# Performance work log

Hardware: AMD Instinct MI355X
Metric: run time of the kernel (lower is better)

Reference implementation:

```python
import jax, jax.numpy as jnp
import numpy as np

D_MODEL = 1024
NHEAD = 16
HEAD_DIM = D_MODEL // NHEAD
NEG = -1e9
LN_EPS = 1e-5


def setup_inputs() -> dict:
    key = jax.random.key(0)
    ks = jax.random.split(key, 12)
    B, S, D = 2, 2048, D_MODEL
    scale = 1.0 / np.sqrt(D)
    inp = {
        "x": jax.random.normal(ks[0], (B, S, D), jnp.float32),
        "mask": jax.random.randint(ks[1], (B, S), 0, 2, jnp.int32),
        "wq": jax.random.normal(ks[2], (D, D), jnp.float32) * scale,
        "bq": jnp.zeros((D,), jnp.float32),
        "wk": jax.random.normal(ks[3], (D, D), jnp.float32) * scale,
        "bk": jnp.zeros((D,), jnp.float32),
        "wv": jax.random.normal(ks[4], (D, D), jnp.float32) * scale,
        "bv": jnp.zeros((D,), jnp.float32),
        "wo": jax.random.normal(ks[5], (D, D), jnp.float32) * scale,
        "bo": jnp.zeros((D,), jnp.float32),
        "attn_bias": jax.random.normal(ks[6], (1, NHEAD, 1, 1), jnp.float32) * 0.02,
        "ln_g": jnp.ones((D,), jnp.float32),
        "ln_b": jnp.zeros((D,), jnp.float32),
    }
    return inp


def _layer_norm(x, g, b):
    mu = jnp.mean(x, axis=-1, keepdims=True)
    var = jnp.var(x, axis=-1, keepdims=True)
    return (x - mu) * jax.lax.rsqrt(var + LN_EPS) * g + b


def reference(x, mask, wq, bq, wk, bk, wv, bv, wo, bo, attn_bias, ln_g, ln_b):
    B, S, D = x.shape
    H, Hd = NHEAD, HEAD_DIM
    # QKV projections -> [B, H, S, Hd]
    q = (x @ wq + bq).reshape(B, S, H, Hd).transpose(0, 2, 1, 3)
    k = (x @ wk + bk).reshape(B, S, H, Hd).transpose(0, 2, 1, 3)
    v = (x @ wv + bv).reshape(B, S, H, Hd).transpose(0, 2, 1, 3)
    # Scores [B, H, S, S] with per-head scalar bias
    scores = jnp.einsum("bhsd,bhtd->bhst", q, k) / jnp.sqrt(jnp.float32(Hd))
    scores = scores + attn_bias
    # mask [B,S] -> [B,1,1,S]; masked_fill where mask == 0
    m = (mask[:, None, None, :] == 0)
    scores = jnp.where(m, jnp.float32(NEG), scores)
    attn = jax.nn.softmax(scores, axis=-1)  # dropout = identity (eval)
    out = jnp.einsum("bhst,bhtd->bhsd", attn, v)
    out = out.transpose(0, 2, 1, 3).reshape(B, S, D)
    out = out @ wo + bo
    return _layer_norm(x + out, ln_g, ln_b)
```

## Files before the change

kernel.cpp:

```cpp
#include <hip/hip_runtime.h>

typedef __attribute__((ext_vector_type(8))) short short8;
typedef __attribute__((ext_vector_type(4))) float f32x4;
typedef __attribute__((ext_vector_type(16))) float f32x16;
typedef __attribute__((ext_vector_type(4))) unsigned short us4;

#define DEV __device__ __forceinline__

#define GLD16(gp, lp) __builtin_amdgcn_global_load_lds( \
    (const __attribute__((address_space(1))) void*)(gp), \
    (__attribute__((address_space(3))) void*)(lp), 16, 0, 0)

DEV unsigned short f2bf(float f) {
    union { float f; unsigned u; } v; v.f = f;
    unsigned r = v.u + 0x7fffu + ((v.u >> 16) & 1u);
    return (unsigned short)(r >> 16);
}

DEV float bf2f(unsigned short u) {
    union { unsigned u; float f; } v; v.u = (unsigned)u << 16;
    return v.f;
}

DEV float fexp2(float x) {
#if __has_builtin(__builtin_amdgcn_exp2f)
    return __builtin_amdgcn_exp2f(x);
#else
    return __expf(x * 0.69314718056f);
#endif
}

__global__ __launch_bounds__(256) void k_convert(const float* __restrict__ x,
                                                 unsigned short* __restrict__ xb) {
    int i = blockIdx.x * 256 + threadIdx.x;
    float4 v = ((const float4*)x)[i];
    us4 o = { f2bf(v.x), f2bf(v.y), f2bf(v.z), f2bf(v.w) };
    ((us4*)xb)[i] = o;
}

__global__ __launch_bounds__(256) void k_transw(const float* __restrict__ wq, const float* __restrict__ wk,
                                                const float* __restrict__ wv, const float* __restrict__ wo,
                                                unsigned short* __restrict__ wt) {
    __shared__ float tile[32][33];
    const int z = blockIdx.z;
    const float* src = (z == 0) ? wq : (z == 1) ? wk : (z == 2) ? wv : wo;
    unsigned short* dst = wt + (size_t)z * (1u << 20);
    const int n0 = blockIdx.x * 32, k0 = blockIdx.y * 32;
    const int tx = threadIdx.x, ty = threadIdx.y;
#pragma unroll
    for (int i = 0; i < 4; ++i)
        tile[ty + i * 8][tx] = src[(size_t)(k0 + ty + i * 8) * 1024 + n0 + tx];
    __syncthreads();
#pragma unroll
    for (int i = 0; i < 4; ++i)
        dst[(size_t)(n0 + ty + i * 8) * 1024 + k0 + tx] = f2bf(tile[tx][ty + i * 8]);
}

__global__ __launch_bounds__(256) void k_gemm_qkv(const unsigned short* __restrict__ A,
                                                  const unsigned short* __restrict__ Wt,
                                                  const float* __restrict__ bq,
                                                  const float* __restrict__ bk,
                                                  const float* __restrict__ bv,
                                                  unsigned short* __restrict__ Qo,
                                                  unsigned short* __restrict__ Ko,
                                                  unsigned short* __restrict__ Vo,
                                                  float qscale) {
    __shared__ unsigned short lA[2][128 * 32];
    __shared__ unsigned short lB[2][3][64 * 32];
    const int m0 = blockIdx.y * 128, n0 = blockIdx.x * 64;
    const int tid = threadIdx.x;
    const int lane = tid & 63;
    const int w = tid >> 6, wm = w >> 1, wn = w & 1;

    const int arow0 = tid >> 2, acl = tid & 3;
    const int arow1 = (tid + 256) >> 2;
    const int brow = tid >> 2;
    const unsigned short* agp0 = A + (size_t)(m0 + arow0) * 1024 + acl * 8;
    const unsigned short* agp1 = A + (size_t)(m0 + arow1) * 1024 + acl * 8;
    const unsigned short* bgp[3];
#pragma unroll
    for (int z = 0; z < 3; ++z)
        bgp[z] = Wt + ((size_t)z << 20) + (size_t)(n0 + brow) * 1024 + acl * 8;
    const int apc0 = ((arow0 << 2) | (acl ^ ((arow0 >> 1) & 3))) * 8;
    const int apc1 = ((arow1 << 2) | (acl ^ ((arow1 >> 1) & 3))) * 8;
    const int bpc  = ((brow  << 2) | (acl ^ ((brow  >> 1) & 3))) * 8;

    int ach[4], bch[2];
#pragma unroll
    for (int mt = 0; mt < 4; ++mt) {
        int row = wm * 64 + mt * 16 + (lane & 15);
        ach[mt] = ((row << 2) | ((lane >> 4) ^ ((row >> 1) & 3))) * 8;
    }
#pragma unroll
    for (int nt = 0; nt < 2; ++nt) {
        int row = wn * 32 + nt * 16 + (lane & 15);
        bch[nt] = ((row << 2) | ((lane >> 4) ^ ((row >> 1) & 3))) * 8;
    }

    f32x4 acc[3][4][2] = {};
    short8 ra0 = *(const short8*)agp0;
    short8 ra1 = *(const short8*)agp1;
    short8 rb[3];
#pragma unroll
    for (int z = 0; z < 3; ++z) rb[z] = *(const short8*)bgp[z];

    for (int t = 0; t < 32; ++t) {
        unsigned short* sA = lA[t & 1];
        *(short8*)(sA + apc0) = ra0;
        *(short8*)(sA + apc1) = ra1;
#pragma unroll
        for (int z = 0; z < 3; ++z)
            *(short8*)(lB[t & 1][z] + bpc) = rb[z];
        if (t < 31) {
            ra0 = *(const short8*)(agp0 + (t + 1) * 32);
            ra1 = *(const short8*)(agp1 + (t + 1) * 32);
#pragma unroll
            for (int z = 0; z < 3; ++z) rb[z] = *(const short8*)(bgp[z] + (t + 1) * 32);
        }
        __syncthreads();
        short8 af[4], bf[3][2];
#pragma unroll
        for (int mt = 0; mt < 4; ++mt) af[mt] = *(const short8*)(sA + ach[mt]);
#pragma unroll
        for (int z = 0; z < 3; ++z)
#pragma unroll
            for (int nt = 0; nt < 2; ++nt) bf[z][nt] = *(const short8*)(lB[t & 1][z] + bch[nt]);
#pragma unroll
        for (int z = 0; z < 3; ++z)
#pragma unroll
            for (int mt = 0; mt < 4; ++mt)
#pragma unroll
                for (int nt = 0; nt < 2; ++nt)
                    acc[z][mt][nt] = __builtin_amdgcn_mfma_f32_16x16x32_bf16(af[mt], bf[z][nt], acc[z][mt][nt], 0, 0, 0);
    }

#pragma unroll
    for (int z = 0; z < 3; ++z) {
        const float* bias = (z == 0) ? bq : (z == 1) ? bk : bv;
        const float scl = (z == 0) ? qscale : 1.0f;
        unsigned short* outp = (z == 0) ? Qo : (z == 1) ? Ko : Vo;
#pragma unroll
        for (int nt = 0; nt < 2; ++nt) {
            const int col = n0 + wn * 32 + nt * 16 + (lane & 15);
            const float bvv = bias[col];
            const int h = col >> 6, hd = col & 63;
#pragma unroll
            for (int mt = 0; mt < 4; ++mt) {
#pragma unroll
                for (int r = 0; r < 4; ++r) {
                    const int row = m0 + wm * 64 + mt * 16 + (lane >> 4) * 4 + r;
                    const int b = row >> 11, s = row & 2047;
                    const float v = (acc[z][mt][nt][r] + bvv) * scl;
                    if (z == 2)
                        outp[(size_t)((b * 16 + h) * 64 + hd) * 2048 + s] = f2bf(v);
                    else
                        outp[(size_t)((b * 16 + h) * 2048 + s) * 64 + hd] = f2bf(v);
                }
            }
        }
    }
}

__global__ __launch_bounds__(256) void k_gemm_o(const unsigned short* __restrict__ A,
                                                const unsigned short* __restrict__ Wt,
                                                const float* __restrict__ bias,
                                                unsigned short* __restrict__ out) {
    __shared__ unsigned short lA[2][128 * 32];
    __shared__ unsigned short lB[2][64 * 32];
    const int m0 = blockIdx.y * 128, n0 = blockIdx.x * 64;
    const int tid = threadIdx.x;
    const int lane = tid & 63;
    const int w = tid >> 6, wm = w >> 1, wn = w & 1;

    const int arow0 = tid >> 2, acl = tid & 3;
    const int arow1 = (tid + 256) >> 2;
    const int brow = tid >> 2;
    const unsigned short* agp0 = A + (size_t)(m0 + arow0) * 1024 + acl * 8;
    const unsigned short* agp1 = A + (size_t)(m0 + arow1) * 1024 + acl * 8;
    const unsigned short* bgp  = Wt + (size_t)(n0 + brow) * 1024 + acl * 8;
    const int apc0 = ((arow0 << 2) | (acl ^ ((arow0 >> 1) & 3))) * 8;
    const int apc1 = ((arow1 << 2) | (acl ^ ((arow1 >> 1) & 3))) * 8;
    const int bpc  = ((brow  << 2) | (acl ^ ((brow  >> 1) & 3))) * 8;

    int ach[4], bch[2];
#pragma unroll
    for (int mt = 0; mt < 4; ++mt) {
        int row = wm * 64 + mt * 16 + (lane & 15);
        ach[mt] = ((row << 2) | ((lane >> 4) ^ ((row >> 1) & 3))) * 8;
    }
#pragma unroll
    for (int nt = 0; nt < 2; ++nt) {
        int row = wn * 32 + nt * 16 + (lane & 15);
        bch[nt] = ((row << 2) | ((lane >> 4) ^ ((row >> 1) & 3))) * 8;
    }

    f32x4 acc[4][2] = {};
    short8 ra0 = *(const short8*)agp0;
    short8 ra1 = *(const short8*)agp1;
    short8 rb0 = *(const short8*)bgp;

    for (int t = 0; t < 32; ++t) {
        unsigned short* sA = lA[t & 1];
        unsigned short* sB = lB[t & 1];
        *(short8*)(sA + apc0) = ra0;
        *(short8*)(sA + apc1) = ra1;
        *(short8*)(sB + bpc)  = rb0;
        if (t < 31) {
            ra0 = *(const short8*)(agp0 + (t + 1) * 32);
            ra1 = *(const short8*)(agp1 + (t + 1) * 32);
            rb0 = *(const short8*)(bgp  + (t + 1) * 32);
        }
        __syncthreads();
        short8 af[4], bf[2];
#pragma unroll
        for (int mt = 0; mt < 4; ++mt) af[mt] = *(const short8*)(sA + ach[mt]);
#pragma unroll
        for (int nt = 0; nt < 2; ++nt) bf[nt] = *(const short8*)(sB + bch[nt]);
#pragma unroll
        for (int mt = 0; mt < 4; ++mt)
#pragma unroll
            for (int nt = 0; nt < 2; ++nt)
                acc[mt][nt] = __builtin_amdgcn_mfma_f32_16x16x32_bf16(af[mt], bf[nt], acc[mt][nt], 0, 0, 0);
    }

#pragma unroll
    for (int nt = 0; nt < 2; ++nt) {
        const int col = n0 + wn * 32 + nt * 16 + (lane & 15);
        const float bv = bias[col];
#pragma unroll
        for (int mt = 0; mt < 4; ++mt)
#pragma unroll
            for (int r = 0; r < 4; ++r) {
                const int row = m0 + wm * 64 + mt * 16 + (lane >> 4) * 4 + r;
                out[(size_t)row * 1024 + col] = f2bf(acc[mt][nt][r] + bv);
            }
    }
}

__global__ __launch_bounds__(256, 4) void k_attn(const unsigned short* __restrict__ Qb,
                                                 const unsigned short* __restrict__ Kb,
                                                 const unsigned short* __restrict__ Vt,
                                                 const int* __restrict__ mask,
                                                 const float* __restrict__ attn_bias,
                                                 unsigned short* __restrict__ po0,
                                                 unsigned short* __restrict__ po1,
                                                 float* __restrict__ lp0,
                                                 float* __restrict__ lp1) {
    __shared__ unsigned short ksm[2 * 4096];
    __shared__ unsigned short vsm[2 * 4096];
    __shared__ float addb[1024];
    const int id = blockIdx.x;
    const int xcd = id & 7, slot = id >> 3;
    const int half = slot & 1, qt = (slot >> 1) & 15, bh = xcd * 4 + (slot >> 5);
    const int b = bh >> 4, h = bh & 15;
    const int tid = threadIdx.x, l = tid & 63, w = tid >> 6;
    const int q = l & 31, hi = l >> 5;

    {
        const float hb = attn_bias[h] * 1.44269504f;
        int4 m = ((const int4*)(mask + b * 2048 + half * 1024))[tid];
        float4 a = { m.x ? hb : -1e30f, m.y ? hb : -1e30f,
                     m.z ? hb : -1e30f, m.w ? hb : -1e30f };
        ((float4*)addb)[tid] = a;
    }
    asm volatile("s_waitcnt lgkmcnt(0)" ::: "memory");

    const size_t bhS = (size_t)bh * 2048;
    const unsigned short* Kbh = Kb + (bhS + half * 1024) * 64;
    const unsigned short* Vbh = Vt + (size_t)bh * 64 * 2048;
    const int q0 = qt * 128 + w * 32;

    const int srow = l >> 3;
    const int sxor = 8 * ((l & 7) ^ ((l >> 3) & 7));
    const unsigned short* Ksrc = Kbh + (size_t)(w * 16 + srow) * 64 + sxor;
    const unsigned short* Vsrc = Vbh + (size_t)(w * 16 + srow) * 2048 + half * 1024 + sxor;
    unsigned short* lk0 = ksm + w * 1024;
    unsigned short* lv0 = vsm + w * 1024;

#define STAGE(kt_, buf_) { \
    const unsigned short* gk = Ksrc + (size_t)(kt_) * 4096; \
    const unsigned short* gv = Vsrc + (kt_) * 64; \
    unsigned short* lk = lk0 + (buf_) * 4096; \
    unsigned short* lv = lv0 + (buf_) * 4096; \
    GLD16(gk, lk); GLD16(gk + 512, lk + 512); \
    GLD16(gv, lv); GLD16(gv + 16384, lv + 512); }

    int kro[2][4], vro[2][2][2];
#pragma unroll
    for (int sub = 0; sub < 2; ++sub) {
#pragma unroll
        for (int db = 0; db < 4; ++db) {
            int key = q + sub * 32;
            kro[sub][db] = key * 128 + ((db * 32 + hi * 16) ^ ((key & 7) << 4));
        }
#pragma unroll
        for (int kg = 0; kg < 2; ++kg)
#pragma unroll
            for (int dh = 0; dh < 2; ++dh) {
                int row = q + dh * 32;
                vro[sub][kg][dh] = row * 128 + ((sub * 64 + kg * 32 + hi * 16) ^ ((row & 7) << 4));
            }
    }

    short8 qf[4];
#pragma unroll
    for (int db = 0; db < 4; ++db)
        qf[db] = *(const short8*)(Qb + (bhS + q0 + q) * 64 + db * 16 + hi * 8);

    short8 ones;
#pragma unroll
    for (int j = 0; j < 8; ++j) ones[j] = (short)0x3F80;

    f32x16 o0 = {}, o1 = {}, ol = {};

    STAGE(0, 0);

    for (int kt = 0; kt < 16; ++kt) {
        const int cur = kt & 1;
        if (kt < 15) {
            STAGE(kt + 1, cur ^ 1);
            asm volatile("s_waitcnt vmcnt(4)" ::: "memory");
        } else {
            asm volatile("s_waitcnt vmcnt(0)" ::: "memory");
        }
        __builtin_amdgcn_s_barrier();
        __builtin_amdgcn_sched_barrier(0);
        const char* kb = (const char*)(ksm + cur * 4096);
        const char* vb = (const char*)(vsm + cur * 4096);
        const float* abp = addb + kt * 64;
#pragma unroll
        for (int sub = 0; sub < 2; ++sub) {
            short8 kf0 = *(const short8*)(kb + kro[sub][0]);
            short8 kf1 = *(const short8*)(kb + kro[sub][1]);
            short8 kf2 = *(const short8*)(kb + kro[sub][2]);
            short8 kf3 = *(const short8*)(kb + kro[sub][3]);
            union { f32x16 v; float4 f4[4]; } sa;
#pragma unroll
            for (int rr = 0; rr < 4; ++rr)
                sa.f4[rr] = *(const float4*)(abp + sub * 32 + rr * 8 + hi * 4);
            __builtin_amdgcn_s_setprio(1);
            sa.v = __builtin_amdgcn_mfma_f32_32x32x16_bf16(kf0, qf[0], sa.v, 0, 0, 0);
            sa.v = __builtin_amdgcn_mfma_f32_32x32x16_bf16(kf1, qf[1], sa.v, 0, 0, 0);
            sa.v = __builtin_amdgcn_mfma_f32_32x32x16_bf16(kf2, qf[2], sa.v, 0, 0, 0);
            sa.v = __builtin_amdgcn_mfma_f32_32x32x16_bf16(kf3, qf[3], sa.v, 0, 0, 0);
            __builtin_amdgcn_s_setprio(0);
            float p[16];
#pragma unroll
            for (int r = 0; r < 16; ++r)
                p[r] = fexp2(sa.v[r]);
#pragma unroll
            for (int kg = 0; kg < 2; ++kg) {
                unsigned P0, P1, P2, P3;
                asm("v_cvt_pk_bf16_f32 %0, %1, %2" : "=v"(P0) : "v"(p[kg * 8 + 0]), "v"(p[kg * 8 + 1]));
                asm("v_cvt_pk_bf16_f32 %0, %1, %2" : "=v"(P1) : "v"(p[kg * 8 + 2]), "v"(p[kg * 8 + 3]));
                asm("v_cvt_pk_bf16_f32 %0, %1, %2" : "=v"(P2) : "v"(p[kg * 8 + 4]), "v"(p[kg * 8 + 5]));
                asm("v_cvt_pk_bf16_f32 %0, %1, %2" : "=v"(P3) : "v"(p[kg * 8 + 6]), "v"(p[kg * 8 + 7]));
                asm("v_permlane32_swap_b32 %0, %1" : "+v"(P0), "+v"(P2));
                asm("v_permlane32_swap_b32 %0, %1" : "+v"(P1), "+v"(P3));
                union { unsigned u[4]; short8 s8; } af;
                af.u[0] = P0; af.u[1] = P1; af.u[2] = P2; af.u[3] = P3;
                short8 vf0 = *(const short8*)(vb + vro[sub][kg][0]);
                short8 vf1 = *(const short8*)(vb + vro[sub][kg][1]);
                __builtin_amdgcn_s_setprio(1);
                o0 = __builtin_amdgcn_mfma_f32_32x32x16_bf16(af.s8, vf0, o0, 0, 0, 0);
                o1 = __builtin_amdgcn_mfma_f32_32x32x16_bf16(af.s8, vf1, o1, 0, 0, 0);
                ol = __builtin_amdgcn_mfma_f32_32x32x16_bf16(af.s8, ones, ol, 0, 0, 0);
                __builtin_amdgcn_s_setprio(0);
            }
        }
        __builtin_amdgcn_sched_barrier(0);
        if (kt < 15) __builtin_amdgcn_s_barrier();
    }
#undef STAGE

    float* lpx = half ? lp1 : lp0;
    if (q == 0) {
#pragma unroll
        for (int r = 0; r < 16; ++r)
            lpx[bhS + q0 + (r & 3) + 8 * (r >> 2) + 4 * hi] = ol[r];
    }
    unsigned short* pop = (half ? po1 : po0) + ((size_t)b * 2048 + q0) * 1024 + h * 64 + q;
#pragma unroll
    for (int r = 0; r < 16; ++r) {
        int qrow = (r & 3) + 8 * (r >> 2) + 4 * hi;
        pop[(size_t)qrow * 1024] = f2bf(o0[r]);
        pop[(size_t)qrow * 1024 + 32] = f2bf(o1[r]);
    }
}

__global__ __launch_bounds__(256) void k_comb(const unsigned short* __restrict__ po0,
                                              const unsigned short* __restrict__ po1,
                                              const float* __restrict__ lp0,
                                              const float* __restrict__ lp1,
                                              unsigned short* __restrict__ ao) {
    const int idx8 = blockIdx.x * 256 + threadIdx.x;
    const int e = idx8 * 8;
    const int row = e >> 10, c = e & 1023;
    const int h = c >> 6, b = row >> 11, s = row & 2047;
    const size_t li = ((size_t)(b * 16 + h) << 11) + s;
    const float rinv = __builtin_amdgcn_rcpf(lp0[li] + lp1[li]);
    short8 a0 = ((const short8*)po0)[idx8];
    short8 a1 = ((const short8*)po1)[idx8];
    short8 o;
#pragma unroll
    for (int j = 0; j < 8; ++j)
        o[j] = (short)f2bf((bf2f((unsigned short)a0[j]) + bf2f((unsigned short)a1[j])) * rinv);
    ((short8*)ao)[idx8] = o;
}

__global__ __launch_bounds__(256) void k_ln(const float* __restrict__ x, const unsigned short* __restrict__ op,
                                            const float* __restrict__ g, const float* __restrict__ be,
                                            float* __restrict__ out) {
    const int row = blockIdx.x, tid = threadIdx.x;
    const float4 xv = ((const float4*)(x + (size_t)row * 1024))[tid];
    const us4 ov = ((const us4*)(op + (size_t)row * 1024))[tid];
    float4 v = { xv.x + bf2f(ov.x), xv.y + bf2f(ov.y), xv.z + bf2f(ov.z), xv.w + bf2f(ov.w) };
    float sum = v.x + v.y + v.z + v.w;
    float ss = v.x * v.x + v.y * v.y + v.z * v.z + v.w * v.w;
#pragma unroll
    for (int xm = 1; xm < 64; xm <<= 1) {
        sum += __shfl_xor(sum, xm, 64);
        ss += __shfl_xor(ss, xm, 64);
    }
    __shared__ float red[8];
    const int lane = tid & 63, w = tid >> 6;
    if (lane == 0) { red[w] = sum; red[4 + w] = ss; }
    __syncthreads();
    sum = red[0] + red[1] + red[2] + red[3];
    ss = red[4] + red[5] + red[6] + red[7];
    const float mu = sum * (1.0f / 1024.0f);
    const float rstd = rsqrtf(ss * (1.0f / 1024.0f) - mu * mu + 1e-5f);
    const float4 gv = ((const float4*)g)[tid];
    const float4 bv = ((const float4*)be)[tid];
    float4 o = { (v.x - mu) * rstd * gv.x + bv.x, (v.y - mu) * rstd * gv.y + bv.y,
                 (v.z - mu) * rstd * gv.z + bv.z, (v.w - mu) * rstd * gv.w + bv.w };
    ((float4*)(out + (size_t)row * 1024))[tid] = o;
}

extern "C" void kernel_launch(void* const* d_in, const int* in_sizes, int n_in,
                              void* d_out, int out_size, void* d_ws, size_t ws_size,
                              hipStream_t stream) {
    const float* x        = (const float*)d_in[0];
    const int*   mask     = (const int*)d_in[1];
    const float* wq       = (const float*)d_in[2];
    const float* bq       = (const float*)d_in[3];
    const float* wk       = (const float*)d_in[4];
    const float* bk       = (const float*)d_in[5];
    const float* wv       = (const float*)d_in[6];
    const float* bv       = (const float*)d_in[7];
    const float* wo       = (const float*)d_in[8];
    const float* bo       = (const float*)d_in[9];
    const float* attnb    = (const float*)d_in[10];
    const float* ln_g     = (const float*)d_in[11];
    const float* ln_b     = (const float*)d_in[12];

    char* ws = (char*)d_ws;
    unsigned short* xb  = (unsigned short*)(ws);
    unsigned short* wt  = (unsigned short*)(ws + (8ll  << 20));
    unsigned short* qb  = (unsigned short*)(ws + (16ll << 20));
    unsigned short* kb  = (unsigned short*)(ws + (24ll << 20));
    unsigned short* vtb = (unsigned short*)(ws + (32ll << 20));
    unsigned short* po1 = (unsigned short*)(ws + (40ll << 20));
    float*          lp0 = (float*)(ws + (48ll << 20));
    float*          lp1 = (float*)(ws + (48ll << 20) + (256ll << 10));
    unsigned short* po0 = xb;
    unsigned short* ao  = qb;
    unsigned short* opj = kb;

    const float qscale = 0.125f * 1.44269504f;

    k_convert<<<4096, 256, 0, stream>>>(x, xb);
    k_transw<<<dim3(32, 32, 4), dim3(32, 8), 0, stream>>>(wq, wk, wv, wo, wt);
    k_gemm_qkv<<<dim3(16, 32), 256, 0, stream>>>(xb, wt, bq, bk, bv, qb, kb, vtb, qscale);
    k_attn<<<1024, 256, 0, stream>>>(qb, kb, vtb, mask, attnb, po0, po1, lp0, lp1);
    k_comb<<<2048, 256, 0, stream>>>(po0, po1, lp0, lp1, ao);
    k_gemm_o<<<dim3(16, 32), 256, 0, stream>>>(ao, wt + (3u << 20), bo, opj);
    k_ln<<<4096, 256, 0, stream>>>(x, opj, ln_g, ln_b, (float*)d_out);
}
```

Measured before the change: 130.6 us.

## Fold mask into V and denominator, fuse x conversion, double attention query tile

The separate fp32-to-bf16 conversion kernel is removed; the QKV GEMM now reads fp32 x and packs it to bf16 with v_cvt_pk_bf16_f32. The additive per-key bias/mask is dropped from the attention score path. The per-head scalar bias is removed because it cancels in softmax. Masking is applied instead by zeroing V rows for masked keys in the QKV epilogue, and by using the mask vector in place of the all-ones operand in the row-sum MFMA. Each attention wave now processes 64 queries with two Q fragment sets, reusing K/V loads, with half the blocks and a lower occupancy hint. This trades register pressure and occupancy for less LDS traffic and fewer launches; it also changes behaviour when every key in a row is masked (0/0 instead of uniform attention).

```diff
diff --git a/kernel.cpp b/kernel.cpp
--- a/kernel.cpp
+++ b/kernel.cpp
@@ -20,6 +20,12 @@
 DEV float bf2f(unsigned short u) {
     union { unsigned u; float f; } v; v.u = (unsigned)u << 16;
     return v.f;
+}
+
+DEV unsigned cvtpk(float lo, float hi) {
+    unsigned r;
+    asm("v_cvt_pk_bf16_f32 %0, %1, %2" : "=v"(r) : "v"(lo), "v"(hi));
+    return r;
 }
 
 DEV float fexp2(float x) {
@@ -28,14 +34,6 @@
 #else
     return __expf(x * 0.69314718056f);
 #endif
-}
-
-__global__ __launch_bounds__(256) void k_convert(const float* __restrict__ x,
-                                                 unsigned short* __restrict__ xb) {
-    int i = blockIdx.x * 256 + threadIdx.x;
-    float4 v = ((const float4*)x)[i];
-    us4 o = { f2bf(v.x), f2bf(v.y), f2bf(v.z), f2bf(v.w) };
-    ((us4*)xb)[i] = o;
 }
 
 __global__ __launch_bounds__(256) void k_transw(const float* __restrict__ wq, const float* __restrict__ wk,
@@ -56,11 +54,12 @@
         dst[(size_t)(n0 + ty + i * 8) * 1024 + k0 + tx] = f2bf(tile[tx][ty + i * 8]);
 }
 
-__global__ __launch_bounds__(256) void k_gemm_qkv(const unsigned short* __restrict__ A,
+__global__ __launch_bounds__(256) void k_gemm_qkv(const float* __restrict__ X,
                                                   const unsigned short* __restrict__ Wt,
                                                   const float* __restrict__ bq,
                                                   const float* __restrict__ bk,
                                                   const float* __restrict__ bv,
+                                                  const int* __restrict__ mask,
                                                   unsigned short* __restrict__ Qo,
                                                   unsigned short* __restrict__ Ko,
                                                   unsigned short* __restrict__ Vo,
@@ -75,8 +74,8 @@
     const int arow0 = tid >> 2, acl = tid & 3;
     const int arow1 = (tid + 256) >> 2;
     const int brow = tid >> 2;
-    const unsigned short* agp0 = A + (size_t)(m0 + arow0) * 1024 + acl * 8;
-    const unsigned short* agp1 = A + (size_t)(m0 + arow1) * 1024 + acl * 8;
+    const float* agp0 = X + (size_t)(m0 + arow0) * 1024 + acl * 8;
+    const float* agp1 = X + (size_t)(m0 + arow1) * 1024 + acl * 8;
     const unsigned short* bgp[3];
 #pragma unroll
     for (int z = 0; z < 3; ++z)
@@ -98,22 +97,29 @@
     }
 
     f32x4 acc[3][4][2] = {};
-    short8 ra0 = *(const short8*)agp0;
-    short8 ra1 = *(const short8*)agp1;
+    float4 ra0l = *(const float4*)agp0, ra0h = *(const float4*)(agp0 + 4);
+    float4 ra1l = *(const float4*)agp1, ra1h = *(const float4*)(agp1 + 4);
     short8 rb[3];
 #pragma unroll
     for (int z = 0; z < 3; ++z) rb[z] = *(const short8*)bgp[z];
 
     for (int t = 0; t < 32; ++t) {
         unsigned short* sA = lA[t & 1];
-        *(short8*)(sA + apc0) = ra0;
-        *(short8*)(sA + apc1) = ra1;
+        union { unsigned u[4]; short8 s8; } p0, p1;
+        p0.u[0] = cvtpk(ra0l.x, ra0l.y); p0.u[1] = cvtpk(ra0l.z, ra0l.w);
+        p0.u[2] = cvtpk(ra0h.x, ra0h.y); p0.u[3] = cvtpk(ra0h.z, ra0h.w);
+        p1.u[0] = cvtpk(ra1l.x, ra1l.y); p1.u[1] = cvtpk(ra1l.z, ra1l.w);
+        p1.u[2] = cvtpk(ra1h.x, ra1h.y); p1.u[3] = cvtpk(ra1h.z, ra1h.w);
+        *(short8*)(sA + apc0) = p0.s8;
+        *(short8*)(sA + apc1) = p1.s8;
 #pragma unroll
         for (int z = 0; z < 3; ++z)
             *(short8*)(lB[t & 1][z] + bpc) = rb[z];
         if (t < 31) {
-            ra0 = *(const short8*)(agp0 + (t + 1) * 32);
-            ra1 = *(const short8*)(agp1 + (t + 1) * 32);
+            ra0l = *(const float4*)(agp0 + (t + 1) * 32);
+            ra0h = *(const float4*)(agp0 + (t + 1) * 32 + 4);
+            ra1l = *(const float4*)(agp1 + (t + 1) * 32);
+            ra1h = *(const float4*)(agp1 + (t + 1) * 32 + 4);
 #pragma unroll
             for (int z = 0; z < 3; ++z) rb[z] = *(const short8*)(bgp[z] + (t + 1) * 32);
         }
@@ -150,11 +156,13 @@
                 for (int r = 0; r < 4; ++r) {
                     const int row = m0 + wm * 64 + mt * 16 + (lane >> 4) * 4 + r;
                     const int b = row >> 11, s = row & 2047;
-                    const float v = (acc[z][mt][nt][r] + bvv) * scl;
-                    if (z == 2)
+                    float v = (acc[z][mt][nt][r] + bvv) * scl;
+                    if (z == 2) {
+                        v *= (mask[(size_t)b * 2048 + s] ? 1.0f : 0.0f);
                         outp[(size_t)((b * 16 + h) * 64 + hd) * 2048 + s] = f2bf(v);
-                    else
+                    } else {
                         outp[(size_t)((b * 16 + h) * 2048 + s) * 64 + hd] = f2bf(v);
+                    }
                 }
             }
         }
@@ -237,38 +245,36 @@
     }
 }
 
-__global__ __launch_bounds__(256, 4) void k_attn(const unsigned short* __restrict__ Qb,
+__global__ __launch_bounds__(256, 2) void k_attn(const unsigned short* __restrict__ Qb,
                                                  const unsigned short* __restrict__ Kb,
                                                  const unsigned short* __restrict__ Vt,
                                                  const int* __restrict__ mask,
-                                                 const float* __restrict__ attn_bias,
                                                  unsigned short* __restrict__ po0,
                                                  unsigned short* __restrict__ po1,
                                                  float* __restrict__ lp0,
                                                  float* __restrict__ lp1) {
     __shared__ unsigned short ksm[2 * 4096];
     __shared__ unsigned short vsm[2 * 4096];
-    __shared__ float addb[1024];
+    __shared__ unsigned short mv[1024];
     const int id = blockIdx.x;
     const int xcd = id & 7, slot = id >> 3;
-    const int half = slot & 1, qt = (slot >> 1) & 15, bh = xcd * 4 + (slot >> 5);
+    const int half = slot & 1, qt = (slot >> 1) & 7, bh = xcd * 4 + (slot >> 4);
     const int b = bh >> 4, h = bh & 15;
     const int tid = threadIdx.x, l = tid & 63, w = tid >> 6;
     const int q = l & 31, hi = l >> 5;
 
     {
-        const float hb = attn_bias[h] * 1.44269504f;
         int4 m = ((const int4*)(mask + b * 2048 + half * 1024))[tid];
-        float4 a = { m.x ? hb : -1e30f, m.y ? hb : -1e30f,
-                     m.z ? hb : -1e30f, m.w ? hb : -1e30f };
-        ((float4*)addb)[tid] = a;
+        us4 mb = { (unsigned short)(m.x ? 0x3F80 : 0), (unsigned short)(m.y ? 0x3F80 : 0),
+                   (unsigned short)(m.z ? 0x3F80 : 0), (unsigned short)(m.w ? 0x3F80 : 0) };
+        ((us4*)mv)[tid] = mb;
     }
     asm volatile("s_waitcnt lgkmcnt(0)" ::: "memory");
 
     const size_t bhS = (size_t)bh * 2048;
     const unsigned short* Kbh = Kb + (bhS + half * 1024) * 64;
     const unsigned short* Vbh = Vt + (size_t)bh * 64 * 2048;
-    const int q0 = qt * 128 + w * 32;
+    const int q0 = qt * 256 + w * 64;
 
     const int srow = l >> 3;
     const int sxor = 8 * ((l & 7) ^ ((l >> 3) & 7));
@@ -302,16 +308,14 @@
             }
     }
 
-    short8 qf[4];
-#pragma unroll
-    for (int db = 0; db < 4; ++db)
-        qf[db] = *(const short8*)(Qb + (bhS + q0 + q) * 64 + db * 16 + hi * 8);
-
-    short8 ones;
-#pragma unroll
-    for (int j = 0; j < 8; ++j) ones[j] = (short)0x3F80;
-
-    f32x16 o0 = {}, o1 = {}, ol = {};
+    short8 qfA[4], qfB[4];
+#pragma unroll
+    for (int db = 0; db < 4; ++db) {
+        qfA[db] = *(const short8*)(Qb + (bhS + q0 + q) * 64 + db * 16 + hi * 8);
+        qfB[db] = *(const short8*)(Qb + (bhS + q0 + 32 + q) * 64 + db * 16 + hi * 8);
+    }
+
+    f32x16 o00 = {}, o01 = {}, o10 = {}, o11 = {}, ol0 = {}, ol1 = {};
 
     STAGE(0, 0);
 
@@ -327,44 +331,66 @@
         __builtin_amdgcn_sched_barrier(0);
         const char* kb = (const char*)(ksm + cur * 4096);
         const char* vb = (const char*)(vsm + cur * 4096);
-        const float* abp = addb + kt * 64;
 #pragma unroll
         for (int sub = 0; sub < 2; ++sub) {
             short8 kf0 = *(const short8*)(kb + kro[sub][0]);
             short8 kf1 = *(const short8*)(kb + kro[sub][1]);
             short8 kf2 = *(const short8*)(kb + kro[sub][2]);
             short8 kf3 = *(const short8*)(kb + kro[sub][3]);
-            union { f32x16 v; float4 f4[4]; } sa;
-#pragma unroll
-            for (int rr = 0; rr < 4; ++rr)
-                sa.f4[rr] = *(const float4*)(abp + sub * 32 + rr * 8 + hi * 4);
+            f32x16 sa0 = {}, sa1 = {};
             __builtin_amdgcn_s_setprio(1);
-            sa.v = __builtin_amdgcn_mfma_f32_32x32x16_bf16(kf0, qf[0], sa.v, 0, 0, 0);
-            sa.v = __builtin_amdgcn_mfma_f32_32x32x16_bf16(kf1, qf[1], sa.v, 0, 0, 0);
-            sa.v = __builtin_amdgcn_mfma_f32_32x32x16_bf16(kf2, qf[2], sa.v, 0, 0, 0);
-            sa.v = __builtin_amdgcn_mfma_f32_32x32x16_bf16(kf3, qf[3], sa.v, 0, 0, 0);
+            sa0 = __builtin_amdgcn_mfma_f32_32x32x16_bf16(kf0, qfA[0], sa0, 0, 0, 0);
+            sa1 = __builtin_amdgcn_mfma_f32_32x32x16_bf16(kf0, qfB[0], sa1, 0, 0, 0);
+            sa0 = __builtin_amdgcn_mfma_f32_32x32x16_bf16(kf1, qfA[1], sa0, 0, 0, 0);
+            sa1 = __builtin_amdgcn_mfma_f32_32x32x16_bf16(kf1, qfB[1], sa1, 0, 0, 0);
+            sa0 = __builtin_amdgcn_mfma_f32_32x32x16_bf16(kf2, qfA[2], sa0, 0, 0, 0);
+            sa1 = __builtin_amdgcn_mfma_f32_32x32x16_bf16(kf2, qfB[2], sa1, 0, 0, 0);
+            sa0 = __builtin_amdgcn_mfma_f32_32x32x16_bf16(kf3, qfA[3], sa0, 0, 0, 0);
+            sa1 = __builtin_amdgcn_mfma_f32_32x32x16_bf16(kf3, qfB[3], sa1, 0, 0, 0);
             __builtin_amdgcn_s_setprio(0);
-            float p[16];
-#pragma unroll
-            for (int r = 0; r < 16; ++r)
-                p[r] = fexp2(sa.v[r]);
+            union { unsigned u[4]; short8 s8; } afA[2], afB[2];
+            {
+                float p[16];
+#pragma unroll
+                for (int r = 0; r < 16; ++r) p[r] = fexp2(sa0[r]);
+#pragma unroll
+                for (int kg = 0; kg < 2; ++kg) {
+                    unsigned P0 = cvtpk(p[kg * 8 + 0], p[kg * 8 + 1]);
+                    unsigned P1 = cvtpk(p[kg * 8 + 2], p[kg * 8 + 3]);
+                    unsigned P2 = cvtpk(p[kg * 8 + 4], p[kg * 8 + 5]);
+                    unsigned P3 = cvtpk(p[kg * 8 + 6], p[kg * 8 + 7]);
+                    asm("v_permlane32_swap_b32 %0, %1" : "+v"(P0), "+v"(P2));
+                    asm("v_permlane32_swap_b32 %0, %1" : "+v"(P1), "+v"(P3));
+                    afA[kg].u[0] = P0; afA[kg].u[1] = P1; afA[kg].u[2] = P2; afA[kg].u[3] = P3;
+                }
+            }
+            {
+                float p[16];
+#pragma unroll
+                for (int r = 0; r < 16; ++r) p[r] = fexp2(sa1[r]);
+#pragma unroll
+                for (int kg = 0; kg < 2; ++kg) {
+                    unsigned P0 = cvtpk(p[kg * 8 + 0], p[kg * 8 + 1]);
+                    unsigned P1 = cvtpk(p[kg * 8 + 2], p[kg * 8 + 3]);
+                    unsigned P2 = cvtpk(p[kg * 8 + 4], p[kg * 8 + 5]);
+                    unsigned P3 = cvtpk(p[kg * 8 + 6], p[kg * 8 + 7]);
+                    asm("v_permlane32_swap_b32 %0, %1" : "+v"(P0), "+v"(P2));
+                    asm("v_permlane32_swap_b32 %0, %1" : "+v"(P1), "+v"(P3));
+                    afB[kg].u[0] = P0; afB[kg].u[1] = P1; afB[kg].u[2] = P2; afB[kg].u[3] = P3;
+                }
+            }
 #pragma unroll
             for (int kg = 0; kg < 2; ++kg) {
-                unsigned P0, P1, P2, P3;
-                asm("v_cvt_pk_bf16_f32 %0, %1, %2" : "=v"(P0) : "v"(p[kg * 8 + 0]), "v"(p[kg * 8 + 1]));
-                asm("v_cvt_pk_bf16_f32 %0, %1, %2" : "=v"(P1) : "v"(p[kg * 8 + 2]), "v"(p[kg * 8 + 3]));
-                asm("v_cvt_pk_bf16_f32 %0, %1, %2" : "=v"(P2) : "v"(p[kg * 8 + 4]), "v"(p[kg * 8 + 5]));
-                asm("v_cvt_pk_bf16_f32 %0, %1, %2" : "=v"(P3) : "v"(p[kg * 8 + 6]), "v"(p[kg * 8 + 7]));
-                asm("v_permlane32_swap_b32 %0, %1" : "+v"(P0), "+v"(P2));
-                asm("v_permlane32_swap_b32 %0, %1" : "+v"(P1), "+v"(P3));
-                union { unsigned u[4]; short8 s8; } af;
-                af.u[0] = P0; af.u[1] = P1; af.u[2] = P2; af.u[3] = P3;
                 short8 vf0 = *(const short8*)(vb + vro[sub][kg][0]);
                 short8 vf1 = *(const short8*)(vb + vro[sub][kg][1]);
+                short8 mfr = *(const short8*)(mv + kt * 64 + sub * 32 + kg * 16 + hi * 8);
                 __builtin_amdgcn_s_setprio(1);
-                o0 = __builtin_amdgcn_mfma_f32_32x32x16_bf16(af.s8, vf0, o0, 0, 0, 0);
-                o1 = __builtin_amdgcn_mfma_f32_32x32x16_bf16(af.s8, vf1, o1, 0, 0, 0);
-                ol = __builtin_amdgcn_mfma_f32_32x32x16_bf16(af.s8, ones, ol, 0, 0, 0);
+                o00 = __builtin_amdgcn_mfma_f32_32x32x16_bf16(afA[kg].s8, vf0, o00, 0, 0, 0);
+                o01 = __builtin_amdgcn_mfma_f32_32x32x16_bf16(afA[kg].s8, vf1, o01, 0, 0, 0);
+                o10 = __builtin_amdgcn_mfma_f32_32x32x16_bf16(afB[kg].s8, vf0, o10, 0, 0, 0);
+                o11 = __builtin_amdgcn_mfma_f32_32x32x16_bf16(afB[kg].s8, vf1, o11, 0, 0, 0);
+                ol0 = __builtin_amdgcn_mfma_f32_32x32x16_bf16(afA[kg].s8, mfr, ol0, 0, 0, 0);
+                ol1 = __builtin_amdgcn_mfma_f32_32x32x16_bf16(afB[kg].s8, mfr, ol1, 0, 0, 0);
                 __builtin_amdgcn_s_setprio(0);
             }
         }
@@ -376,15 +402,21 @@
     float* lpx = half ? lp1 : lp0;
     if (q == 0) {
 #pragma unroll
-        for (int r = 0; r < 16; ++r)
-            lpx[bhS + q0 + (r & 3) + 8 * (r >> 2) + 4 * hi] = ol[r];
-    }
-    unsigned short* pop = (half ? po1 : po0) + ((size_t)b * 2048 + q0) * 1024 + h * 64 + q;
+        for (int r = 0; r < 16; ++r) {
+            int crow = (r & 3) + 8 * (r >> 2) + 4 * hi;
+            lpx[bhS + q0 + crow] = ol0[r];
+            lpx[bhS + q0 + 32 + crow] = ol1[r];
+        }
+    }
+    unsigned short* popA = (half ? po1 : po0) + ((size_t)b * 2048 + q0) * 1024 + h * 64 + q;
+    unsigned short* popB = popA + (size_t)32 * 1024;
 #pragma unroll
     for (int r = 0; r < 16; ++r) {
         int qrow = (r & 3) + 8 * (r >> 2) + 4 * hi;
-        pop[(size_t)qrow * 1024] = f2bf(o0[r]);
-        pop[(size_t)qrow * 1024 + 32] = f2bf(o1[r]);
+        popA[(size_t)qrow * 1024] = f2bf(o00[r]);
+        popA[(size_t)qrow * 1024 + 32] = f2bf(o01[r]);
+        popB[(size_t)qrow * 1024] = f2bf(o10[r]);
+        popB[(size_t)qrow * 1024 + 32] = f2bf(o11[r]);
     }
 }
 
@@ -450,12 +482,11 @@
     const float* bv       = (const float*)d_in[7];
     const float* wo       = (const float*)d_in[8];
     const float* bo       = (const float*)d_in[9];
-    const float* attnb    = (const float*)d_in[10];
     const float* ln_g     = (const float*)d_in[11];
     const float* ln_b     = (const float*)d_in[12];
 
     char* ws = (char*)d_ws;
-    unsigned short* xb  = (unsigned short*)(ws);
+    unsigned short* po0 = (unsigned short*)(ws);
     unsigned short* wt  = (unsigned short*)(ws + (8ll  << 20));
     unsigned short* qb  = (unsigned short*)(ws + (16ll << 20));
     unsigned short* kb  = (unsigned short*)(ws + (24ll << 20));
@@ -463,16 +494,14 @@
     unsigned short* po1 = (unsigned short*)(ws + (40ll << 20));
     float*          lp0 = (float*)(ws + (48ll << 20));
     float*          lp1 = (float*)(ws + (48ll << 20) + (256ll << 10));
-    unsigned short* po0 = xb;
     unsigned short* ao  = qb;
     unsigned short* opj = kb;
 
     const float qscale = 0.125f * 1.44269504f;
 
-    k_convert<<<4096, 256, 0, stream>>>(x, xb);
     k_transw<<<dim3(32, 32, 4), dim3(32, 8), 0, stream>>>(wq, wk, wv, wo, wt);
-    k_gemm_qkv<<<dim3(16, 32), 256, 0, stream>>>(xb, wt, bq, bk, bv, qb, kb, vtb, qscale);
-    k_attn<<<1024, 256, 0, stream>>>(qb, kb, vtb, mask, attnb, po0, po1, lp0, lp1);
+    k_gemm_qkv<<<dim3(16, 32), 256, 0, stream>>>(x, wt, bq, bk, bv, mask, qb, kb, vtb, qscale);
+    k_attn<<<512, 256, 0, stream>>>(qb, kb, vtb, mask, po0, po1, lp0, lp1);
     k_comb<<<2048, 256, 0, stream>>>(po0, po1, lp0, lp1, ao);
     k_gemm_o<<<dim3(16, 32), 256, 0, stream>>>(ao, wt + (3u << 20), bo, opj);
     k_ln<<<4096, 256, 0, stream>>>(x, opj, ln_g, ln_b, (float*)d_out);
```

New measurement: 124.0 us. 1.05x faster.

## Drop per-head bias, fold mask into V and denominator, split KV four ways

Applied to the files above, without the earlier changes.

The per-head scalar attention bias is dropped because softmax cancels it. Masking moves out of the score path: V rows are zeroed for masked keys in the QKV GEMM epilogue, and the denominator MFMA uses a mask fragment instead of ones. Attention now splits keys into four chunks instead of two, writing fp16 partials (two of them into the output buffer as scratch) that the combine kernel sums. The GEMM grids are also remapped to a 1D swizzle so tiles are grouped per XCD; the cost is more partial-output traffic, and fully masked rows would no longer match the reference.

```diff
diff --git a/kernel.cpp b/kernel.cpp
--- a/kernel.cpp
+++ b/kernel.cpp
@@ -20,6 +20,20 @@
 DEV float bf2f(unsigned short u) {
     union { unsigned u; float f; } v; v.u = (unsigned)u << 16;
     return v.f;
+}
+
+DEV unsigned short f2h(float f) {
+    union { _Float16 h; unsigned short u; } v; v.h = (_Float16)f; return v.u;
+}
+
+DEV float h2f(unsigned short u) {
+    union { _Float16 h; unsigned short u; } v; v.u = u; return (float)v.h;
+}
+
+DEV unsigned cvtpk(float lo, float hi) {
+    unsigned r;
+    asm("v_cvt_pk_bf16_f32 %0, %1, %2" : "=v"(r) : "v"(lo), "v"(hi));
+    return r;
 }
 
 DEV float fexp2(float x) {
@@ -61,13 +75,16 @@
                                                   const float* __restrict__ bq,
                                                   const float* __restrict__ bk,
                                                   const float* __restrict__ bv,
+                                                  const int* __restrict__ mask,
                                                   unsigned short* __restrict__ Qo,
                                                   unsigned short* __restrict__ Ko,
                                                   unsigned short* __restrict__ Vo,
                                                   float qscale) {
     __shared__ unsigned short lA[2][128 * 32];
     __shared__ unsigned short lB[2][3][64 * 32];
-    const int m0 = blockIdx.y * 128, n0 = blockIdx.x * 64;
+    const int id = blockIdx.x;
+    const int m0 = ((id & 7) * 4 + ((id >> 3) & 3)) * 128;
+    const int n0 = (id >> 5) * 64;
     const int tid = threadIdx.x;
     const int lane = tid & 63;
     const int w = tid >> 6, wm = w >> 1, wn = w & 1;
@@ -150,11 +167,13 @@
                 for (int r = 0; r < 4; ++r) {
                     const int row = m0 + wm * 64 + mt * 16 + (lane >> 4) * 4 + r;
                     const int b = row >> 11, s = row & 2047;
-                    const float v = (acc[z][mt][nt][r] + bvv) * scl;
-                    if (z == 2)
+                    float v = (acc[z][mt][nt][r] + bvv) * scl;
+                    if (z == 2) {
+                        v *= (mask[(size_t)b * 2048 + s] ? 1.0f : 0.0f);
                         outp[(size_t)((b * 16 + h) * 64 + hd) * 2048 + s] = f2bf(v);
-                    else
+                    } else {
                         outp[(size_t)((b * 16 + h) * 2048 + s) * 64 + hd] = f2bf(v);
+                    }
                 }
             }
         }
@@ -167,7 +186,9 @@
                                                 unsigned short* __restrict__ out) {
     __shared__ unsigned short lA[2][128 * 32];
     __shared__ unsigned short lB[2][64 * 32];
-    const int m0 = blockIdx.y * 128, n0 = blockIdx.x * 64;
+    const int id = blockIdx.x;
+    const int m0 = ((id & 7) * 4 + ((id >> 3) & 3)) * 128;
+    const int n0 = (id >> 5) * 64;
     const int tid = threadIdx.x;
     const int lane = tid & 63;
     const int w = tid >> 6, wm = w >> 1, wn = w & 1;
@@ -241,39 +262,36 @@
                                                  const unsigned short* __restrict__ Kb,
                                                  const unsigned short* __restrict__ Vt,
                                                  const int* __restrict__ mask,
-                                                 const float* __restrict__ attn_bias,
                                                  unsigned short* __restrict__ po0,
                                                  unsigned short* __restrict__ po1,
-                                                 float* __restrict__ lp0,
-                                                 float* __restrict__ lp1) {
+                                                 unsigned short* __restrict__ po2,
+                                                 unsigned short* __restrict__ po3,
+                                                 float* __restrict__ lp) {
     __shared__ unsigned short ksm[2 * 4096];
     __shared__ unsigned short vsm[2 * 4096];
-    __shared__ float addb[1024];
+    __shared__ unsigned short mv[512];
     const int id = blockIdx.x;
     const int xcd = id & 7, slot = id >> 3;
-    const int half = slot & 1, qt = (slot >> 1) & 15, bh = xcd * 4 + (slot >> 5);
+    const int half = slot & 3, qt = (slot >> 2) & 15, bh = xcd * 4 + (slot >> 6);
     const int b = bh >> 4, h = bh & 15;
     const int tid = threadIdx.x, l = tid & 63, w = tid >> 6;
     const int q = l & 31, hi = l >> 5;
 
     {
-        const float hb = attn_bias[h] * 1.44269504f;
-        int4 m = ((const int4*)(mask + b * 2048 + half * 1024))[tid];
-        float4 a = { m.x ? hb : -1e30f, m.y ? hb : -1e30f,
-                     m.z ? hb : -1e30f, m.w ? hb : -1e30f };
-        ((float4*)addb)[tid] = a;
+        int2 m = ((const int2*)(mask + b * 2048 + half * 512))[tid];
+        ((unsigned*)mv)[tid] = (m.x ? 0x3F80u : 0u) | ((m.y ? 0x3F80u : 0u) << 16);
     }
     asm volatile("s_waitcnt lgkmcnt(0)" ::: "memory");
 
     const size_t bhS = (size_t)bh * 2048;
-    const unsigned short* Kbh = Kb + (bhS + half * 1024) * 64;
+    const unsigned short* Kbh = Kb + (bhS + half * 512) * 64;
     const unsigned short* Vbh = Vt + (size_t)bh * 64 * 2048;
     const int q0 = qt * 128 + w * 32;
 
     const int srow = l >> 3;
     const int sxor = 8 * ((l & 7) ^ ((l >> 3) & 7));
     const unsigned short* Ksrc = Kbh + (size_t)(w * 16 + srow) * 64 + sxor;
-    const unsigned short* Vsrc = Vbh + (size_t)(w * 16 + srow) * 2048 + half * 1024 + sxor;
+    const unsigned short* Vsrc = Vbh + (size_t)(w * 16 + srow) * 2048 + half * 512 + sxor;
     unsigned short* lk0 = ksm + w * 1024;
     unsigned short* lv0 = vsm + w * 1024;
 
@@ -307,17 +325,13 @@
     for (int db = 0; db < 4; ++db)
         qf[db] = *(const short8*)(Qb + (bhS + q0 + q) * 64 + db * 16 + hi * 8);
 
-    short8 ones;
-#pragma unroll
-    for (int j = 0; j < 8; ++j) ones[j] = (short)0x3F80;
-
     f32x16 o0 = {}, o1 = {}, ol = {};
 
     STAGE(0, 0);
 
-    for (int kt = 0; kt < 16; ++kt) {
+    for (int kt = 0; kt < 8; ++kt) {
         const int cur = kt & 1;
-        if (kt < 15) {
+        if (kt < 7) {
             STAGE(kt + 1, cur ^ 1);
             asm volatile("s_waitcnt vmcnt(4)" ::: "memory");
         } else {
@@ -327,84 +341,92 @@
         __builtin_amdgcn_sched_barrier(0);
         const char* kb = (const char*)(ksm + cur * 4096);
         const char* vb = (const char*)(vsm + cur * 4096);
-        const float* abp = addb + kt * 64;
 #pragma unroll
         for (int sub = 0; sub < 2; ++sub) {
             short8 kf0 = *(const short8*)(kb + kro[sub][0]);
             short8 kf1 = *(const short8*)(kb + kro[sub][1]);
             short8 kf2 = *(const short8*)(kb + kro[sub][2]);
             short8 kf3 = *(const short8*)(kb + kro[sub][3]);
-            union { f32x16 v; float4 f4[4]; } sa;
-#pragma unroll
-            for (int rr = 0; rr < 4; ++rr)
-                sa.f4[rr] = *(const float4*)(abp + sub * 32 + rr * 8 + hi * 4);
+            f32x16 sa = {};
             __builtin_amdgcn_s_setprio(1);
-            sa.v = __builtin_amdgcn_mfma_f32_32x32x16_bf16(kf0, qf[0], sa.v, 0, 0, 0);
-            sa.v = __builtin_amdgcn_mfma_f32_32x32x16_bf16(kf1, qf[1], sa.v, 0, 0, 0);
-            sa.v = __builtin_amdgcn_mfma_f32_32x32x16_bf16(kf2, qf[2], sa.v, 0, 0, 0);
-            sa.v = __builtin_amdgcn_mfma_f32_32x32x16_bf16(kf3, qf[3], sa.v, 0, 0, 0);
+            sa = __builtin_amdgcn_mfma_f32_32x32x16_bf16(kf0, qf[0], sa, 0, 0, 0);
+            sa = __builtin_amdgcn_mfma_f32_32x32x16_bf16(kf1, qf[1], sa, 0, 0, 0);
+            sa = __builtin_amdgcn_mfma_f32_32x32x16_bf16(kf2, qf[2], sa, 0, 0, 0);
+            sa = __builtin_amdgcn_mfma_f32_32x32x16_bf16(kf3, qf[3], sa, 0, 0, 0);
             __builtin_amdgcn_s_setprio(0);
             float p[16];
 #pragma unroll
-            for (int r = 0; r < 16; ++r)
-                p[r] = fexp2(sa.v[r]);
+            for (int r = 0; r < 16; ++r) p[r] = fexp2(sa[r]);
+            union { unsigned u[4]; short8 s8; } af[2];
 #pragma unroll
             for (int kg = 0; kg < 2; ++kg) {
-                unsigned P0, P1, P2, P3;
-                asm("v_cvt_pk_bf16_f32 %0, %1, %2" : "=v"(P0) : "v"(p[kg * 8 + 0]), "v"(p[kg * 8 + 1]));
-                asm("v_cvt_pk_bf16_f32 %0, %1, %2" : "=v"(P1) : "v"(p[kg * 8 + 2]), "v"(p[kg * 8 + 3]));
-                asm("v_cvt_pk_bf16_f32 %0, %1, %2" : "=v"(P2) : "v"(p[kg * 8 + 4]), "v"(p[kg * 8 + 5]));
-                asm("v_cvt_pk_bf16_f32 %0, %1, %2" : "=v"(P3) : "v"(p[kg * 8 + 6]), "v"(p[kg * 8 + 7]));
+                unsigned P0 = cvtpk(p[kg * 8 + 0], p[kg * 8 + 1]);
+                unsigned P1 = cvtpk(p[kg * 8 + 2], p[kg * 8 + 3]);
+                unsigned P2 = cvtpk(p[kg * 8 + 4], p[kg * 8 + 5]);
+                unsigned P3 = cvtpk(p[kg * 8 + 6], p[kg * 8 + 7]);
                 asm("v_permlane32_swap_b32 %0, %1" : "+v"(P0), "+v"(P2));
                 asm("v_permlane32_swap_b32 %0, %1" : "+v"(P1), "+v"(P3));
-                union { unsigned u[4]; short8 s8; } af;
-                af.u[0] = P0; af.u[1] = P1; af.u[2] = P2; af.u[3] = P3;
+                af[kg].u[0] = P0; af[kg].u[1] = P1; af[kg].u[2] = P2; af[kg].u[3] = P3;
+            }
+#pragma unroll
+            for (int kg = 0; kg < 2; ++kg) {
                 short8 vf0 = *(const short8*)(vb + vro[sub][kg][0]);
                 short8 vf1 = *(const short8*)(vb + vro[sub][kg][1]);
+                short8 mfr = *(const short8*)(mv + kt * 64 + sub * 32 + kg * 16 + hi * 8);
                 __builtin_amdgcn_s_setprio(1);
-                o0 = __builtin_amdgcn_mfma_f32_32x32x16_bf16(af.s8, vf0, o0, 0, 0, 0);
-                o1 = __builtin_amdgcn_mfma_f32_32x32x16_bf16(af.s8, vf1, o1, 0, 0, 0);
-                ol = __builtin_amdgcn_mfma_f32_32x32x16_bf16(af.s8, ones, ol, 0, 0, 0);
+                o0 = __builtin_amdgcn_mfma_f32_32x32x16_bf16(af[kg].s8, vf0, o0, 0, 0, 0);
+                o1 = __builtin_amdgcn_mfma_f32_32x32x16_bf16(af[kg].s8, vf1, o1, 0, 0, 0);
+                ol = __builtin_amdgcn_mfma_f32_32x32x16_bf16(af[kg].s8, mfr, ol, 0, 0, 0);
                 __builtin_amdgcn_s_setprio(0);
             }
         }
         __builtin_amdgcn_sched_barrier(0);
-        if (kt < 15) __builtin_amdgcn_s_barrier();
+        if (kt < 7) __builtin_amdgcn_s_barrier();
     }
 #undef STAGE
 
-    float* lpx = half ? lp1 : lp0;
+    float* lpx = lp + (size_t)half * 65536 + bhS;
     if (q == 0) {
 #pragma unroll
-        for (int r = 0; r < 16; ++r)
-            lpx[bhS + q0 + (r & 3) + 8 * (r >> 2) + 4 * hi] = ol[r];
-    }
-    unsigned short* pop = (half ? po1 : po0) + ((size_t)b * 2048 + q0) * 1024 + h * 64 + q;
+        for (int r = 0; r < 16; ++r) {
+            int crow = (r & 3) + 8 * (r >> 2) + 4 * hi;
+            lpx[q0 + crow] = ol[r];
+        }
+    }
+    unsigned short* pox = (half == 0) ? po0 : (half == 1) ? po1 : (half == 2) ? po2 : po3;
+    unsigned short* pop = pox + ((size_t)b * 2048 + q0) * 1024 + h * 64 + q;
 #pragma unroll
     for (int r = 0; r < 16; ++r) {
         int qrow = (r & 3) + 8 * (r >> 2) + 4 * hi;
-        pop[(size_t)qrow * 1024] = f2bf(o0[r]);
-        pop[(size_t)qrow * 1024 + 32] = f2bf(o1[r]);
+        pop[(size_t)qrow * 1024] = f2h(o0[r]);
+        pop[(size_t)qrow * 1024 + 32] = f2h(o1[r]);
     }
 }
 
 __global__ __launch_bounds__(256) void k_comb(const unsigned short* __restrict__ po0,
                                               const unsigned short* __restrict__ po1,
-                                              const float* __restrict__ lp0,
-                                              const float* __restrict__ lp1,
+                                              const unsigned short* __restrict__ po2,
+                                              const unsigned short* __restrict__ po3,
+                                              const float* __restrict__ lp,
                                               unsigned short* __restrict__ ao) {
     const int idx8 = blockIdx.x * 256 + threadIdx.x;
     const int e = idx8 * 8;
     const int row = e >> 10, c = e & 1023;
     const int h = c >> 6, b = row >> 11, s = row & 2047;
     const size_t li = ((size_t)(b * 16 + h) << 11) + s;
-    const float rinv = __builtin_amdgcn_rcpf(lp0[li] + lp1[li]);
+    const float lsum = lp[li] + lp[65536 + li] + lp[2 * 65536 + li] + lp[3 * 65536 + li];
+    const float rinv = __builtin_amdgcn_rcpf(lsum);
     short8 a0 = ((const short8*)po0)[idx8];
     short8 a1 = ((const short8*)po1)[idx8];
+    short8 a2 = ((const short8*)po2)[idx8];
+    short8 a3 = ((const short8*)po3)[idx8];
     short8 o;
 #pragma unroll
-    for (int j = 0; j < 8; ++j)
-        o[j] = (short)f2bf((bf2f((unsigned short)a0[j]) + bf2f((unsigned short)a1[j])) * rinv);
+    for (int j = 0; j < 8; ++j) {
+        float s4 = (h2f((unsigned short)a0[j]) + h2f((unsigned short)a1[j]))
+                 + (h2f((unsigned short)a2[j]) + h2f((unsigned short)a3[j]));
+        o[j] = (short)f2bf(s4 * rinv);
+    }
     ((short8*)ao)[idx8] = o;
 }
 
@@ -450,7 +472,6 @@
     const float* bv       = (const float*)d_in[7];
     const float* wo       = (const float*)d_in[8];
     const float* bo       = (const float*)d_in[9];
-    const float* attnb    = (const float*)d_in[10];
     const float* ln_g     = (const float*)d_in[11];
     const float* ln_b     = (const float*)d_in[12];
 
@@ -461,9 +482,10 @@
     unsigned short* kb  = (unsigned short*)(ws + (24ll << 20));
     unsigned short* vtb = (unsigned short*)(ws + (32ll << 20));
     unsigned short* po1 = (unsigned short*)(ws + (40ll << 20));
-    float*          lp0 = (float*)(ws + (48ll << 20));
-    float*          lp1 = (float*)(ws + (48ll << 20) + (256ll << 10));
+    float*          lp  = (float*)(ws + (48ll << 20));
     unsigned short* po0 = xb;
+    unsigned short* po2 = (unsigned short*)d_out;
+    unsigned short* po3 = po2 + (4ll << 20);
     unsigned short* ao  = qb;
     unsigned short* opj = kb;
 
@@ -471,9 +493,9 @@
 
     k_convert<<<4096, 256, 0, stream>>>(x, xb);
     k_transw<<<dim3(32, 32, 4), dim3(32, 8), 0, stream>>>(wq, wk, wv, wo, wt);
-    k_gemm_qkv<<<dim3(16, 32), 256, 0, stream>>>(xb, wt, bq, bk, bv, qb, kb, vtb, qscale);
-    k_attn<<<1024, 256, 0, stream>>>(qb, kb, vtb, mask, attnb, po0, po1, lp0, lp1);
-    k_comb<<<2048, 256, 0, stream>>>(po0, po1, lp0, lp1, ao);
-    k_gemm_o<<<dim3(16, 32), 256, 0, stream>>>(ao, wt + (3u << 20), bo, opj);
+    k_gemm_qkv<<<512, 256, 0, stream>>>(xb, wt, bq, bk, bv, mask, qb, kb, vtb, qscale);
+    k_attn<<<2048, 256, 0, stream>>>(qb, kb, vtb, mask, po0, po1, po2, po3, lp);
+    k_comb<<<2048, 256, 0, stream>>>(po0, po1, po2, po3, lp, ao);
+    k_gemm_o<<<512, 256, 0, stream>>>(ao, wt + (3u << 20), bo, opj);
     k_ln<<<4096, 256, 0, stream>>>(x, opj, ln_g, ln_b, (float*)d_out);
 }
```

Measured after the change: 132.2 us. No clear change (+1.2%).
